# Kernel tuning notes

Measured on AMD Instinct MI355X. Metric: run time of the kernel, lower is better.

## Reference

```python
import jax, jax.numpy as jnp
import numpy as np
import math

KSIZE = 4  # ShortConvolution kernel_size
EPS_NORM = 1e-12
EPS_LN = 1e-5


def short_conv(x, w):
    # x: [b, l, c]; w: [c, K] depthwise causal conv + residual (y = conv(pad(x)) + x)
    b, l, c = x.shape
    K = w.shape[1]
    xp = jnp.pad(x, ((0, 0), (K - 1, 0), (0, 0)))
    y = x  # residual term (x[:, :, K-1:] after padding == x)
    for j in range(K):
        y = y + xp[:, j:j + l, :] * w[:, j]
    return y


def l2norm(x):
    # L2-normalize over last dim (interpreting torch.norm as F.normalize intent)
    return x * jax.lax.rsqrt(jnp.sum(x * x, axis=-1, keepdims=True) + EPS_NORM)


def setup_inputs() -> dict:
    key = jax.random.key(0)
    ks = jax.random.split(key, 12)
    b, l, dim = 4, 2048, 1024
    h = 16
    dk = dim // h
    s = 1.0 / math.sqrt(dim)
    inp = {
        "hidden_states": jax.random.normal(ks[0], (b, l, dim), jnp.float32),
        "Wq": jax.random.normal(ks[1], (dim, dim), jnp.float32) * s,
        "Wk": jax.random.normal(ks[2], (dim, dim), jnp.float32) * s,
        "Wv": jax.random.normal(ks[3], (dim, dim), jnp.float32) * s,
        "conv_q": jax.random.normal(ks[4], (dim, KSIZE), jnp.float32) * 0.1,
        "conv_k": jax.random.normal(ks[5], (dim, KSIZE), jnp.float32) * 0.1,
        "conv_v": jax.random.normal(ks[6], (dim, KSIZE), jnp.float32) * 0.1,
        "W_init": jax.random.normal(ks[7], (1, h, dk, dk), jnp.float32) / math.sqrt(dk),
        "ln_gamma": jnp.ones((dk,), jnp.float32),
        "ln_beta": jnp.zeros((dk,), jnp.float32),
        "Wg": jax.random.normal(ks[8], (dim, dim), jnp.float32) * s,
        "Wo": jax.random.normal(ks[9], (dim, dim), jnp.float32) * s,
    }
    return inp


def titans_forward(hidden_states, Wq, Wk, Wv, conv_q, conv_k, conv_v,
                   W_init, ln_gamma, ln_beta, Wg, Wo,
                   num_heads=16, chunk_size=16):
    b, l, dim = hidden_states.shape
    h = num_heads
    dk = dim // h
    cs = chunk_size
    nc = l // cs

    q = l2norm(jax.nn.silu(short_conv(hidden_states @ Wq.T, conv_q)).reshape(b, l, h, dk))
    k = l2norm(jax.nn.silu(short_conv(hidden_states @ Wk.T, conv_k)).reshape(b, l, h, dk))
    v = jax.nn.silu(short_conv(hidden_states @ Wv.T, conv_v)).reshape(b, l, h, dk)

    # chunked layout: [nc, b, cs, h, d]
    qc = q.reshape(b, nc, cs, h, dk).transpose(1, 0, 2, 3, 4)
    kc = k.reshape(b, nc, cs, h, dk).transpose(1, 0, 2, 3, 4)
    vc = v.reshape(b, nc, cs, h, dk).transpose(1, 0, 2, 3, 4)

    mask = jnp.tril(jnp.ones((cs, cs), q.dtype))
    W0 = jnp.broadcast_to(W_init, (b, h, dk, dk))

    def step(W, chunk):
        q_c, k_c, v_c = chunk
        inter = jnp.einsum('bqhk,bhkv->bqhv', q_c, W)
        qk = jnp.einsum('bqhd,bkhd->bhqk', q_c, k_c) * mask
        intra = jnp.einsum('bhqk,bkhv->bqhv', qk, v_c)
        W_new = W + jnp.einsum('bchk,bchv->bhkv', k_c, v_c)
        return W_new, inter + intra

    _, o = jax.lax.scan(step, W0, (qc, kc, vc))  # o: [nc, b, cs, h, dv]
    o = o.transpose(1, 0, 2, 3, 4).reshape(b, l, h, dk)

    # LayerNorm over head_v_dim
    mu = jnp.mean(o, axis=-1, keepdims=True)
    var = jnp.mean((o - mu) ** 2, axis=-1, keepdims=True)
    o = (o - mu) * jax.lax.rsqrt(var + EPS_LN) * ln_gamma + ln_beta

    o = o.reshape(b, l, dim)
    gate = hidden_states @ Wg.T
    return (o * gate) @ Wo.T


def reference(hidden_states, Wq, Wk, Wv, conv_q, conv_k, conv_v,
              W_init, ln_gamma, ln_beta, Wg, Wo):
    return titans_forward(hidden_states, Wq, Wk, Wv, conv_q, conv_k, conv_v,
                          W_init, ln_gamma, ln_beta, Wg, Wo)
```

## Files before the change

### kernel.cpp

```cpp
#include <hip/hip_runtime.h>

#define L 2048
#define DIM 1024
#define ROWS 8192
#define NSEG 16
#define SEG_CHUNKS 8
#define SEG_TOK 128

typedef __attribute__((ext_vector_type(4))) _Float16 v4h;
typedef __attribute__((ext_vector_type(4))) float v4f;
typedef __attribute__((ext_vector_type(8))) short v8s;

#if defined(__HIP_DEVICE_COMPILE__)
#define MFMA_F16_16x16x16(a, b, c) __builtin_amdgcn_mfma_f32_16x16x16f16((a), (b), (c), 0, 0, 0)
#define MFMA_BF16_16x16x32(a, b, c) __builtin_amdgcn_mfma_f32_16x16x32_bf16((a), (b), (c), 0, 0, 0)
#else
#define MFMA_F16_16x16x16(a, b, c) (c)
#define MFMA_BF16_16x16x32(a, b, c) (c)
#endif

__device__ inline void gld16(const unsigned short* g, unsigned short* l) {
#if defined(__HIP_DEVICE_COMPILE__)
  __builtin_amdgcn_global_load_lds(
      (__attribute__((address_space(1))) void*)g,
      (__attribute__((address_space(3))) void*)l, 16, 0, 0);
#endif
}

__device__ inline unsigned short f2bf(float f) {
  unsigned int u = __float_as_uint(f);
  unsigned int r = (u + 0x7fffu + ((u >> 16) & 1u)) >> 16;
  return (unsigned short)r;
}
__device__ inline void u2_unpack(const uint2 u, float* f) {
  f[0] = __uint_as_float((u.x & 0xffffu) << 16);
  f[1] = __uint_as_float(u.x & 0xffff0000u);
  f[2] = __uint_as_float((u.y & 0xffffu) << 16);
  f[3] = __uint_as_float(u.y & 0xffff0000u);
}
__device__ inline uint4 pack8(const float4 a, const float4 b) {
  uint4 u;
  u.x = (unsigned int)f2bf(a.x) | ((unsigned int)f2bf(a.y) << 16);
  u.y = (unsigned int)f2bf(a.z) | ((unsigned int)f2bf(a.w) << 16);
  u.z = (unsigned int)f2bf(b.x) | ((unsigned int)f2bf(b.y) << 16);
  u.w = (unsigned int)f2bf(b.z) | ((unsigned int)f2bf(b.w) << 16);
  return u;
}
__device__ inline unsigned short f2h_us(float f) {
  _Float16 h = (_Float16)f;
  unsigned short u;
  __builtin_memcpy(&u, &h, 2);
  return u;
}
__device__ inline float h2f_us(unsigned short u) {
  _Float16 h;
  __builtin_memcpy(&h, &u, 2);
  return (float)h;
}
__device__ inline void h4_unpack(const uint2 u, float* f) {
  f[0] = h2f_us((unsigned short)(u.x & 0xffffu));
  f[1] = h2f_us((unsigned short)(u.x >> 16));
  f[2] = h2f_us((unsigned short)(u.y & 0xffffu));
  f[3] = h2f_us((unsigned short)(u.y >> 16));
}

__global__ __launch_bounds__(256) void cvt_f2b(const float* __restrict__ s,
                                               unsigned short* __restrict__ d) {
  const int i = blockIdx.x * 256 + threadIdx.x;
  const float4 v = ((const float4*)s)[i];
  uint2 u;
  u.x = (unsigned int)f2bf(v.x) | ((unsigned int)f2bf(v.y) << 16);
  u.y = (unsigned int)f2bf(v.z) | ((unsigned int)f2bf(v.w) << 16);
  ((uint2*)d)[i] = u;
}

__global__ __launch_bounds__(256) void cvt_w4(const float* __restrict__ w0,
                                              const float* __restrict__ w1,
                                              const float* __restrict__ w2,
                                              const float* __restrict__ w3,
                                              unsigned short* __restrict__ dst) {
  const int t = blockIdx.x >> 10;
  const int i = (blockIdx.x & 1023) * 256 + threadIdx.x;
  const float* s = (t == 0) ? w0 : (t == 1) ? w1 : (t == 2) ? w2 : w3;
  const float4 v = ((const float4*)s)[i];
  uint2 u;
  u.x = (unsigned int)f2bf(v.x) | ((unsigned int)f2bf(v.y) << 16);
  u.y = (unsigned int)f2bf(v.z) | ((unsigned int)f2bf(v.w) << 16);
  ((uint2*)(dst + (size_t)t * DIM * DIM))[i] = u;
}

template <int OUTF32>
__global__ __launch_bounds__(256) void gemm_a(const unsigned short* __restrict__ A,
                                              const unsigned short* __restrict__ B,
                                              void* __restrict__ Cv) {
  __shared__ __align__(16) unsigned short As[128 * 64];
  __shared__ __align__(16) unsigned short Bs[128 * 64];
  const int tid = threadIdx.x;
  const int bm = blockIdx.y * 128;
  const int bn = blockIdx.x * 128;
  const int wave = tid >> 6;
  const int lane = tid & 63;
  const int m16 = lane & 15;
  const int g = lane >> 4;
  const int wm = (wave >> 1) * 64;
  const int wn = (wave & 1) * 64;
  const int srow8 = lane >> 3;
  const int schk = lane & 7;

  v4f acc[4][4];
#pragma unroll
  for (int i = 0; i < 4; i++)
#pragma unroll
    for (int j = 0; j < 4; j++) acc[i][j] = (v4f){0.f, 0.f, 0.f, 0.f};

  for (int kt = 0; kt < DIM; kt += 64) {
    __syncthreads();
#pragma unroll
    for (int j = 0; j < 4; j++) {
      const int r = wave * 32 + j * 8 + srow8;
      const int cg = schk ^ (r & 7);
      gld16(A + (size_t)(bm + r) * DIM + kt + cg * 8, &As[(wave * 32 + j * 8) * 64]);
      gld16(B + (size_t)(bn + r) * DIM + kt + cg * 8, &Bs[(wave * 32 + j * 8) * 64]);
    }
    __syncthreads();
#pragma unroll
    for (int kh = 0; kh < 2; kh++) {
      v8s af[4], bf[4];
#pragma unroll
      for (int i = 0; i < 4; i++) {
        const int r = wm + i * 16 + m16;
        af[i] = *(const v8s*)&As[r * 64 + (((kh * 4 + g) ^ (r & 7)) * 8)];
      }
#pragma unroll
      for (int j = 0; j < 4; j++) {
        const int r = wn + j * 16 + m16;
        bf[j] = *(const v8s*)&Bs[r * 64 + (((kh * 4 + g) ^ (r & 7)) * 8)];
      }
#pragma unroll
      for (int i = 0; i < 4; i++)
#pragma unroll
        for (int j = 0; j < 4; j++) acc[i][j] = MFMA_BF16_16x16x32(af[i], bf[j], acc[i][j]);
    }
  }

  const int t = bn >> 10;
  const int cb = bn & 1023;
#pragma unroll
  for (int i = 0; i < 4; i++)
#pragma unroll
    for (int e = 0; e < 4; e++) {
      const size_t row = (size_t)(bm + wm + i * 16 + 4 * g + e);
#pragma unroll
      for (int j = 0; j < 4; j++) {
        const size_t idx = row * DIM + cb + wn + j * 16 + m16;
        if (OUTF32)
          ((float*)Cv)[idx] = acc[i][j][e];
        else
          ((unsigned short*)Cv)[(size_t)t * ((size_t)ROWS * DIM) + idx] = f2bf(acc[i][j][e]);
      }
    }
}

__global__ __launch_bounds__(256) void gemm_gate(const float* __restrict__ Af,
                                                 const unsigned short* __restrict__ Bf,
                                                 unsigned short* __restrict__ C) {
  __shared__ __align__(16) unsigned short As[128][40];
  __shared__ __align__(16) unsigned short Bs[128][40];
  const int tid = threadIdx.x;
  const int bm = blockIdx.y * 128;
  const int bn = blockIdx.x * 128;
  const int wave = tid >> 6;
  const int lane = tid & 63;
  const int m16 = lane & 15;
  const int g = lane >> 4;
  const int wm = (wave >> 1) * 64;
  const int wn = (wave & 1) * 64;
  const int lr = tid >> 2;
  const int lc = (tid & 3) * 8;

  v4f acc[4][4];
#pragma unroll
  for (int i = 0; i < 4; i++)
#pragma unroll
    for (int j = 0; j < 4; j++) acc[i][j] = (v4f){0.f, 0.f, 0.f, 0.f};

  auto loadAB = [&](int kt, uint4& a0, uint4& a1, uint4& b0, uint4& b1) {
    const float* p0 = Af + (size_t)(bm + lr) * DIM + lc + kt;
    const float* p1 = Af + (size_t)(bm + 64 + lr) * DIM + lc + kt;
    a0 = pack8(*(const float4*)p0, *(const float4*)(p0 + 4));
    a1 = pack8(*(const float4*)p1, *(const float4*)(p1 + 4));
    b0 = *(const uint4*)(Bf + (size_t)(bn + lr) * DIM + lc + kt);
    b1 = *(const uint4*)(Bf + (size_t)(bn + 64 + lr) * DIM + lc + kt);
  };

  uint4 a0, a1, b0, b1;
  loadAB(0, a0, a1, b0, b1);

  for (int kt = 0; kt < DIM; kt += 32) {
    __syncthreads();
    *(uint4*)&As[lr][lc] = a0;
    *(uint4*)&As[64 + lr][lc] = a1;
    *(uint4*)&Bs[lr][lc] = b0;
    *(uint4*)&Bs[64 + lr][lc] = b1;
    __syncthreads();
    if (kt + 32 < DIM) loadAB(kt + 32, a0, a1, b0, b1);
    v8s af[4], bf[4];
#pragma unroll
    for (int i = 0; i < 4; i++) af[i] = *(const v8s*)&As[wm + i * 16 + m16][g * 8];
#pragma unroll
    for (int j = 0; j < 4; j++) bf[j] = *(const v8s*)&Bs[wn + j * 16 + m16][g * 8];
#pragma unroll
    for (int i = 0; i < 4; i++)
#pragma unroll
      for (int j = 0; j < 4; j++) acc[i][j] = MFMA_BF16_16x16x32(af[i], bf[j], acc[i][j]);
  }

#pragma unroll
  for (int i = 0; i < 4; i++)
#pragma unroll
    for (int e = 0; e < 4; e++) {
      const size_t row = (size_t)(bm + wm + i * 16 + 4 * g + e);
#pragma unroll
      for (int j = 0; j < 4; j++)
        C[row * DIM + bn + wn + j * 16 + m16] = f2bf(acc[i][j][e]);
    }
}

__global__ __launch_bounds__(256) void copy_side(const unsigned short* __restrict__ Q,
                                                 const unsigned short* __restrict__ K,
                                                 const unsigned short* __restrict__ V,
                                                 unsigned short* __restrict__ sQ,
                                                 unsigned short* __restrict__ sK,
                                                 unsigned short* __restrict__ sV) {
  const int idx = blockIdx.x;
  const int j = idx % 3;
  const int bs = idx / 3;
  const int seg = bs & 15;
  const int b = bs >> 4;
  const int ch = threadIdx.x * 4;
  const size_t so = ((size_t)(bs * 3 + j)) * DIM + ch;
  if (seg == 0) {
    const uint2 z = {0u, 0u};
    *(uint2*)(sQ + so) = z;
    *(uint2*)(sK + so) = z;
    *(uint2*)(sV + so) = z;
  } else {
    const size_t go = ((size_t)(b * L + seg * SEG_TOK - 3 + j)) * DIM + ch;
    *(uint2*)(sQ + so) = *(const uint2*)(Q + go);
    *(uint2*)(sK + so) = *(const uint2*)(K + go);
    *(uint2*)(sV + so) = *(const uint2*)(V + go);
  }
}

__global__ __launch_bounds__(256) void scan_seg(unsigned short* __restrict__ Qr,
                                                const unsigned short* __restrict__ Kr,
                                                unsigned short* __restrict__ Vr,
                                                const unsigned short* __restrict__ sQ,
                                                const unsigned short* __restrict__ sK,
                                                const unsigned short* __restrict__ sV,
                                                const float* __restrict__ CWq,
                                                const float* __restrict__ CWk,
                                                const float* __restrict__ CWv,
                                                float* __restrict__ D) {
  const int seg = blockIdx.x & 15;
  const int h = (blockIdx.x >> 4) & 15;
  const int b = blockIdx.x >> 8;
  const int tid = threadIdx.x;
  const int lane = tid & 63;
  const int dt = tid >> 6;
  const int m = lane & 15;
  const int g = lane >> 4;
  const int segbase = seg * SEG_TOK;

  __shared__ __align__(16) unsigned short rq[32][68];
  __shared__ __align__(16) unsigned short rk[32][68];
  __shared__ __align__(16) unsigned short rv[32][68];
  __shared__ __align__(16) _Float16 qs[16][72];
  __shared__ __align__(16) _Float16 ks[16][72];
  __shared__ __align__(16) _Float16 kts[64][20];
  __shared__ __align__(16) _Float16 vts[64][20];

  v4f Wf[4];
#pragma unroll
  for (int kt = 0; kt < 4; kt++) Wf[kt] = (v4f){0.f, 0.f, 0.f, 0.f};

  const int srow = tid >> 4;
  const int scol = (tid & 15) * 4;
  const size_t gcol = (size_t)h * 64 + scol;

  float wq[4][4], wk[4][4], wv[4][4];
#pragma unroll
  for (int e = 0; e < 4; e++) {
    const float4 a = *(const float4*)(CWq + (gcol + e) * 4);
    const float4 bw = *(const float4*)(CWk + (gcol + e) * 4);
    const float4 cw = *(const float4*)(CWv + (gcol + e) * 4);
    wq[e][0] = a.x; wq[e][1] = a.y; wq[e][2] = a.z; wq[e][3] = a.w;
    wk[e][0] = bw.x; wk[e][1] = bw.y; wk[e][2] = bw.z; wk[e][3] = bw.w;
    wv[e][0] = cw.x; wv[e][1] = cw.y; wv[e][2] = cw.z; wv[e][3] = cw.w;
  }

  if (tid < 48) {
    const int j = tid >> 4;
    const int sc = (tid & 15) * 4;
    const size_t so = ((size_t)((b * NSEG + seg) * 3 + j)) * DIM + h * 64 + sc;
    const int slot = (29 + j);
    *(uint2*)&rq[slot][sc] = *(const uint2*)(sQ + so);
    *(uint2*)&rk[slot][sc] = *(const uint2*)(sK + so);
    *(uint2*)&rv[slot][sc] = *(const uint2*)(sV + so);
  }

  size_t gb = ((size_t)(b * L + segbase + srow)) * DIM + gcol;
  uint2 qg = *(const uint2*)(Qr + gb);
  uint2 kg = *(const uint2*)(Kr + gb);
  uint2 vg = *(const uint2*)(Vr + gb);

  for (int c = 0; c < SEG_CHUNKS; c++) {
    const int t = segbase + c * 16 + srow;
    __syncthreads();
    *(uint2*)&rq[t & 31][scol] = qg;
    *(uint2*)&rk[t & 31][scol] = kg;
    *(uint2*)&rv[t & 31][scol] = vg;
    const int cn = (c + 1 < SEG_CHUNKS) ? c + 1 : c;
    const size_t gbn = ((size_t)(b * L + segbase + cn * 16 + srow)) * DIM + gcol;
    const uint2 qn = *(const uint2*)(Qr + gbn);
    const uint2 kn = *(const uint2*)(Kr + gbn);
    const uint2 vn = *(const uint2*)(Vr + gbn);
    __syncthreads();

    float sq[4], sk[4], sv[4];
    {
      float q0[4], q1[4], q2[4], q3[4];
      float k0[4], k1[4], k2[4], k3[4];
      float v0[4], v1[4], v2[4], v3[4];
      u2_unpack(qg, q0);
      u2_unpack(kg, k0);
      u2_unpack(vg, v0);
      u2_unpack(*(const uint2*)&rq[(t - 1) & 31][scol], q1);
      u2_unpack(*(const uint2*)&rk[(t - 1) & 31][scol], k1);
      u2_unpack(*(const uint2*)&rv[(t - 1) & 31][scol], v1);
      u2_unpack(*(const uint2*)&rq[(t - 2) & 31][scol], q2);
      u2_unpack(*(const uint2*)&rk[(t - 2) & 31][scol], k2);
      u2_unpack(*(const uint2*)&rv[(t - 2) & 31][scol], v2);
      u2_unpack(*(const uint2*)&rq[(t - 3) & 31][scol], q3);
      u2_unpack(*(const uint2*)&rk[(t - 3) & 31][scol], k3);
      u2_unpack(*(const uint2*)&rv[(t - 3) & 31][scol], v3);
#pragma unroll
      for (int e = 0; e < 4; e++) {
        const float yq = q0[e] + wq[e][0] * q3[e] + wq[e][1] * q2[e] + wq[e][2] * q1[e] + wq[e][3] * q0[e];
        const float yk = k0[e] + wk[e][0] * k3[e] + wk[e][1] * k2[e] + wk[e][2] * k1[e] + wk[e][3] * k0[e];
        const float yv = v0[e] + wv[e][0] * v3[e] + wv[e][1] * v2[e] + wv[e][2] * v1[e] + wv[e][3] * v0[e];
        sq[e] = yq / (1.f + __expf(-yq));
        sk[e] = yk / (1.f + __expf(-yk));
        sv[e] = yv / (1.f + __expf(-yv));
      }
    }
    float ssq = sq[0] * sq[0] + sq[1] * sq[1] + sq[2] * sq[2] + sq[3] * sq[3];
    float ssk = sk[0] * sk[0] + sk[1] * sk[1] + sk[2] * sk[2] + sk[3] * sk[3];
#pragma unroll
    for (int off = 8; off >= 1; off >>= 1) {
      ssq += __shfl_xor(ssq, off, 16);
      ssk += __shfl_xor(ssk, off, 16);
    }
    const float scq = rsqrtf(ssq + 1e-12f);
    const float sck = rsqrtf(ssk + 1e-12f);

    const v4h qh = {(_Float16)(sq[0] * scq), (_Float16)(sq[1] * scq),
                    (_Float16)(sq[2] * scq), (_Float16)(sq[3] * scq)};
    const v4h kh = {(_Float16)(sk[0] * sck), (_Float16)(sk[1] * sck),
                    (_Float16)(sk[2] * sck), (_Float16)(sk[3] * sck)};
    *(v4h*)&qs[srow][scol] = qh;
    *(v4h*)&ks[srow][scol] = kh;
    kts[scol + 0][srow] = kh[0]; kts[scol + 1][srow] = kh[1];
    kts[scol + 2][srow] = kh[2]; kts[scol + 3][srow] = kh[3];
    vts[scol + 0][srow] = (_Float16)sv[0]; vts[scol + 1][srow] = (_Float16)sv[1];
    vts[scol + 2][srow] = (_Float16)sv[2]; vts[scol + 3][srow] = (_Float16)sv[3];

    uint2 qp;
    __builtin_memcpy(&qp, &qh, 8);
    *(uint2*)(Qr + gb) = qp;

    __syncthreads();

    v4h qf[4], kf[4], ktf[4];
#pragma unroll
    for (int kt = 0; kt < 4; kt++) {
      qf[kt] = *(const v4h*)&qs[m][kt * 16 + 4 * g];
      kf[kt] = *(const v4h*)&ks[m][kt * 16 + 4 * g];
      ktf[kt] = *(const v4h*)&kts[kt * 16 + m][4 * g];
    }
    const v4h vf = *(const v4h*)&vts[dt * 16 + m][4 * g];

    v4f kq = {0.f, 0.f, 0.f, 0.f};
#pragma unroll
    for (int kt = 0; kt < 4; kt++) kq = MFMA_F16_16x16x16(kf[kt], qf[kt], kq);

    v4h kqA;
#pragma unroll
    for (int e = 0; e < 4; e++)
      kqA[e] = (4 * g + e <= m) ? (_Float16)kq[e] : (_Float16)0.f;

    v4f of = {0.f, 0.f, 0.f, 0.f};
    of = MFMA_F16_16x16x16(kqA, vf, of);
#pragma unroll
    for (int kt = 0; kt < 4; kt++) {
      v4h Wh;
#pragma unroll
      for (int e = 0; e < 4; e++) Wh[e] = (_Float16)Wf[kt][e];
      of = MFMA_F16_16x16x16(qf[kt], Wh, of);
    }
#pragma unroll
    for (int kt = 0; kt < 4; kt++) Wf[kt] = MFMA_F16_16x16x16(ktf[kt], vf, Wf[kt]);

    const size_t ob = ((size_t)(b * L + segbase + c * 16 + 4 * g)) * DIM + h * 64 + dt * 16 + m;
#pragma unroll
    for (int e = 0; e < 4; e++) Vr[ob + (size_t)e * DIM] = f2h_us(of[e]);

    qg = qn; kg = kn; vg = vn; gb = gbn;
  }

  float* Dp = D + ((size_t)((b * 16 + h) * NSEG + seg)) * 4096;
#pragma unroll
  for (int kt = 0; kt < 4; kt++)
#pragma unroll
    for (int e = 0; e < 4; e++)
      Dp[(kt * 16 + 4 * g + e) * 64 + dt * 16 + m] = Wf[kt][e];
}

__global__ __launch_bounds__(256) void prefix_D(float* __restrict__ D,
                                                const float* __restrict__ W0) {
  const int bh = blockIdx.x;
  const int h = bh & 15;
  const int tid = threadIdx.x;
  float p[16];
#pragma unroll
  for (int i = 0; i < 16; i++) p[i] = W0[(size_t)h * 4096 + tid + i * 256];
  for (int s = 0; s < NSEG; s++) {
    float* Dp = D + ((size_t)bh * NSEG + s) * 4096;
#pragma unroll
    for (int i = 0; i < 16; i++) {
      const float t = Dp[tid + i * 256];
      Dp[tid + i * 256] = p[i];
      p[i] += t;
    }
  }
}

__global__ __launch_bounds__(256) void apply_corr(const unsigned short* __restrict__ Qc,
                                                  const float* __restrict__ P,
                                                  unsigned short* __restrict__ Op) {
  const int seg = blockIdx.x & 15;
  const int h = (blockIdx.x >> 4) & 15;
  const int b = blockIdx.x >> 8;
  const int tid = threadIdx.x;
  const int lane = tid & 63;
  const int dt = tid >> 6;
  const int m = lane & 15;
  const int g = lane >> 4;

  __shared__ __align__(16) _Float16 Pt[64][72];
  __shared__ __align__(16) _Float16 qt[16][72];

  const float* Pp = P + ((size_t)((b * 16 + h) * NSEG + seg)) * 4096;
#pragma unroll
  for (int i = 0; i < 16; i++) {
    const int el = tid + i * 256;
    Pt[el & 63][el >> 6] = (_Float16)Pp[el];
  }
  __syncthreads();

  v4h pb[4];
#pragma unroll
  for (int kt = 0; kt < 4; kt++) pb[kt] = *(const v4h*)&Pt[dt * 16 + m][kt * 16 + 4 * g];

  const int srow = tid >> 4;
  const int scol = (tid & 15) * 4;
  for (int rt = 0; rt < 8; rt++) {
    const size_t gb = ((size_t)(b * L + seg * SEG_TOK + rt * 16 + srow)) * DIM + h * 64 + scol;
    const uint2 qg = *(const uint2*)(Qc + gb);
    __syncthreads();
    *(uint2*)&qt[srow][scol] = qg;
    __syncthreads();
    v4h qf[4];
#pragma unroll
    for (int kt = 0; kt < 4; kt++) qf[kt] = *(const v4h*)&qt[m][kt * 16 + 4 * g];
    v4f corr = {0.f, 0.f, 0.f, 0.f};
#pragma unroll
    for (int kt = 0; kt < 4; kt++) corr = MFMA_F16_16x16x16(qf[kt], pb[kt], corr);
    const size_t ob = ((size_t)(b * L + seg * SEG_TOK + rt * 16 + 4 * g)) * DIM + h * 64 + dt * 16 + m;
#pragma unroll
    for (int e = 0; e < 4; e++) {
      const float v = h2f_us(Op[ob + (size_t)e * DIM]) + corr[e];
      Op[ob + (size_t)e * DIM] = f2h_us(v);
    }
  }
}

__global__ __launch_bounds__(256) void ln_gate(unsigned short* __restrict__ Ob,
                                               const unsigned short* __restrict__ G,
                                               const float* __restrict__ gamma,
                                               const float* __restrict__ beta) {
  const int r = blockIdx.x;
  const int tid = threadIdx.x;
  const int c = tid * 4;
  float o[4];
  h4_unpack(*(const uint2*)(Ob + (size_t)r * DIM + c), o);
  float sum = o[0] + o[1] + o[2] + o[3];
#pragma unroll
  for (int off = 8; off >= 1; off >>= 1) sum += __shfl_xor(sum, off, 16);
  const float mu = sum * (1.f / 64.f);
  float d[4];
  float vs = 0.f;
#pragma unroll
  for (int e = 0; e < 4; e++) { d[e] = o[e] - mu; vs += d[e] * d[e]; }
#pragma unroll
  for (int off = 8; off >= 1; off >>= 1) vs += __shfl_xor(vs, off, 16);
  const float rstd = rsqrtf(vs * (1.f / 64.f) + 1e-5f);
  const int dl = c & 63;
  const float4 gm = *(const float4*)(gamma + dl);
  const float4 bt = *(const float4*)(beta + dl);
  float gt[4];
  u2_unpack(*(const uint2*)(G + (size_t)r * DIM + c), gt);
  float outv[4];
  outv[0] = (d[0] * rstd * gm.x + bt.x) * gt[0];
  outv[1] = (d[1] * rstd * gm.y + bt.y) * gt[1];
  outv[2] = (d[2] * rstd * gm.z + bt.z) * gt[2];
  outv[3] = (d[3] * rstd * gm.w + bt.w) * gt[3];
  uint2 u;
  u.x = (unsigned int)f2bf(outv[0]) | ((unsigned int)f2bf(outv[1]) << 16);
  u.y = (unsigned int)f2bf(outv[2]) | ((unsigned int)f2bf(outv[3]) << 16);
  *(uint2*)(Ob + (size_t)r * DIM + c) = u;
}

extern "C" void kernel_launch(void* const* d_in, const int* in_sizes, int n_in,
                              void* d_out, int out_size, void* d_ws, size_t ws_size,
                              hipStream_t stream) {
  const float* H  = (const float*)d_in[0];
  const float* Wq = (const float*)d_in[1];
  const float* Wk = (const float*)d_in[2];
  const float* Wv = (const float*)d_in[3];
  const float* cq = (const float*)d_in[4];
  const float* ck = (const float*)d_in[5];
  const float* cv = (const float*)d_in[6];
  const float* W0 = (const float*)d_in[7];
  const float* gamma = (const float*)d_in[8];
  const float* beta  = (const float*)d_in[9];
  const float* Wg = (const float*)d_in[10];
  const float* Wo = (const float*)d_in[11];

  const size_t SZ = (size_t)ROWS * DIM;
  const size_t WSZ = (size_t)DIM * DIM;
  unsigned short* sA = (unsigned short*)d_ws;
  unsigned short* sB = sA + SZ;
  unsigned short* sC = sB + SZ;

  unsigned short* Hbf = (unsigned short*)d_out;
  unsigned short* Wbf = Hbf + SZ;
  unsigned short* side = Wbf + 4 * WSZ;
  unsigned short* sideQ = side;
  unsigned short* sideK = side + (size_t)192 * DIM;
  unsigned short* sideV = side + (size_t)384 * DIM;
  float* D = (float*)d_out;

  cvt_f2b<<<SZ / 1024, 256, 0, stream>>>(H, Hbf);
  cvt_w4<<<4096, 256, 0, stream>>>(Wq, Wk, Wv, Wg, Wbf);

  gemm_a<0><<<dim3(24, 64), 256, 0, stream>>>(Hbf, Wbf, sA);

  copy_side<<<192, 256, 0, stream>>>(sA, sB, sC, sideQ, sideK, sideV);

  scan_seg<<<1024, 256, 0, stream>>>(sA, sB, sC, sideQ, sideK, sideV,
                                     cq, ck, cv, D);

  gemm_gate<<<dim3(8, 64), 256, 0, stream>>>(H, Wbf + 3 * WSZ, sB);

  prefix_D<<<64, 256, 0, stream>>>(D, W0);

  apply_corr<<<1024, 256, 0, stream>>>(sA, D, sC);

  ln_gate<<<ROWS, 256, 0, stream>>>(sC, sB, gamma, beta);

  cvt_f2b<<<WSZ / 1024, 256, 0, stream>>>(Wo, sA);

  gemm_a<1><<<dim3(8, 64), 256, 0, stream>>>(sC, sA, d_out);
}
```

Baseline: 323.7 us.

## Fuse gate GEMM into QKV GEMM, merge conversions, fuse correction with LayerNorm-gate

Merges the input and weight bf16 conversions into one kernel. When workspace is large enough, computes the gate projection as a fourth output tile group of the bf16 QKV GEMM instead of a separate fp32-input GEMM. Fuses the inter-segment correction with the LayerNorm and gating step, staging corrected outputs in shared memory so the O tensor is not re-read by a separate kernel. This adds more barriers per tile and a workspace-size-dependent code path.

```diff
diff --git a/kernel.cpp b/kernel.cpp
--- a/kernel.cpp
+++ b/kernel.cpp
@@ -62,6 +62,33 @@
   f[1] = h2f_us((unsigned short)(u.x >> 16));
   f[2] = h2f_us((unsigned short)(u.y & 0xffffu));
   f[3] = h2f_us((unsigned short)(u.y >> 16));
+}
+
+__global__ __launch_bounds__(256) void cvt_all(const float* __restrict__ H,
+                                               const float* __restrict__ w0,
+                                               const float* __restrict__ w1,
+                                               const float* __restrict__ w2,
+                                               const float* __restrict__ w3,
+                                               unsigned short* __restrict__ Hbf,
+                                               unsigned short* __restrict__ Wbf) {
+  const int i = blockIdx.x * 256 + threadIdx.x;
+  const float* s;
+  unsigned short* d;
+  int li;
+  if (i < 2097152) {
+    s = H; d = Hbf; li = i;
+  } else {
+    const int j = i - 2097152;
+    const int w = j >> 18;
+    li = j & 262143;
+    s = (w == 0) ? w0 : (w == 1) ? w1 : (w == 2) ? w2 : w3;
+    d = Wbf + (size_t)w * DIM * DIM;
+  }
+  const float4 v = ((const float4*)s)[li];
+  uint2 u;
+  u.x = (unsigned int)f2bf(v.x) | ((unsigned int)f2bf(v.y) << 16);
+  u.y = (unsigned int)f2bf(v.z) | ((unsigned int)f2bf(v.w) << 16);
+  ((uint2*)d)[li] = u;
 }
 
 __global__ __launch_bounds__(256) void cvt_f2b(const float* __restrict__ s,
@@ -74,25 +101,13 @@
   ((uint2*)d)[i] = u;
 }
 
-__global__ __launch_bounds__(256) void cvt_w4(const float* __restrict__ w0,
-                                              const float* __restrict__ w1,
-                                              const float* __restrict__ w2,
-                                              const float* __restrict__ w3,
-                                              unsigned short* __restrict__ dst) {
-  const int t = blockIdx.x >> 10;
-  const int i = (blockIdx.x & 1023) * 256 + threadIdx.x;
-  const float* s = (t == 0) ? w0 : (t == 1) ? w1 : (t == 2) ? w2 : w3;
-  const float4 v = ((const float4*)s)[i];
-  uint2 u;
-  u.x = (unsigned int)f2bf(v.x) | ((unsigned int)f2bf(v.y) << 16);
-  u.y = (unsigned int)f2bf(v.z) | ((unsigned int)f2bf(v.w) << 16);
-  ((uint2*)(dst + (size_t)t * DIM * DIM))[i] = u;
-}
-
 template <int OUTF32>
 __global__ __launch_bounds__(256) void gemm_a(const unsigned short* __restrict__ A,
                                               const unsigned short* __restrict__ B,
-                                              void* __restrict__ Cv) {
+                                              unsigned short* __restrict__ o0,
+                                              unsigned short* __restrict__ o1,
+                                              unsigned short* __restrict__ o2,
+                                              unsigned short* __restrict__ o3) {
   __shared__ __align__(16) unsigned short As[128 * 64];
   __shared__ __align__(16) unsigned short Bs[128 * 64];
   const int tid = threadIdx.x;
@@ -145,6 +160,7 @@
 
   const int t = bn >> 10;
   const int cb = bn & 1023;
+  unsigned short* C = (t == 0) ? o0 : (t == 1) ? o1 : (t == 2) ? o2 : o3;
 #pragma unroll
   for (int i = 0; i < 4; i++)
 #pragma unroll
@@ -154,9 +170,9 @@
       for (int j = 0; j < 4; j++) {
         const size_t idx = row * DIM + cb + wn + j * 16 + m16;
         if (OUTF32)
-          ((float*)Cv)[idx] = acc[i][j][e];
+          ((float*)o0)[idx] = acc[i][j][e];
         else
-          ((unsigned short*)Cv)[(size_t)t * ((size_t)ROWS * DIM) + idx] = f2bf(acc[i][j][e]);
+          C[idx] = f2bf(acc[i][j][e]);
       }
     }
 }
@@ -445,9 +461,12 @@
   }
 }
 
-__global__ __launch_bounds__(256) void apply_corr(const unsigned short* __restrict__ Qc,
-                                                  const float* __restrict__ P,
-                                                  unsigned short* __restrict__ Op) {
+__global__ __launch_bounds__(256) void corr_ln_gate(const unsigned short* __restrict__ Qc,
+                                                    const float* __restrict__ P,
+                                                    unsigned short* __restrict__ Op,
+                                                    const unsigned short* __restrict__ G,
+                                                    const float* __restrict__ gamma,
+                                                    const float* __restrict__ beta) {
   const int seg = blockIdx.x & 15;
   const int h = (blockIdx.x >> 4) & 15;
   const int b = blockIdx.x >> 8;
@@ -459,6 +478,7 @@
 
   __shared__ __align__(16) _Float16 Pt[64][72];
   __shared__ __align__(16) _Float16 qt[16][72];
+  __shared__ __align__(16) float ot[16][68];
 
   const float* Pp = P + ((size_t)((b * 16 + h) * NSEG + seg)) * 4096;
 #pragma unroll
@@ -474,8 +494,12 @@
 
   const int srow = tid >> 4;
   const int scol = (tid & 15) * 4;
+  const float4 gm = *(const float4*)(gamma + scol);
+  const float4 bt = *(const float4*)(beta + scol);
+
   for (int rt = 0; rt < 8; rt++) {
-    const size_t gb = ((size_t)(b * L + seg * SEG_TOK + rt * 16 + srow)) * DIM + h * 64 + scol;
+    const int row0 = seg * SEG_TOK + rt * 16;
+    const size_t gb = ((size_t)(b * L + row0 + srow)) * DIM + h * 64 + scol;
     const uint2 qg = *(const uint2*)(Qc + gb);
     __syncthreads();
     *(uint2*)&qt[srow][scol] = qg;
@@ -486,49 +510,33 @@
     v4f corr = {0.f, 0.f, 0.f, 0.f};
 #pragma unroll
     for (int kt = 0; kt < 4; kt++) corr = MFMA_F16_16x16x16(qf[kt], pb[kt], corr);
-    const size_t ob = ((size_t)(b * L + seg * SEG_TOK + rt * 16 + 4 * g)) * DIM + h * 64 + dt * 16 + m;
-#pragma unroll
-    for (int e = 0; e < 4; e++) {
-      const float v = h2f_us(Op[ob + (size_t)e * DIM]) + corr[e];
-      Op[ob + (size_t)e * DIM] = f2h_us(v);
-    }
-  }
-}
-
-__global__ __launch_bounds__(256) void ln_gate(unsigned short* __restrict__ Ob,
-                                               const unsigned short* __restrict__ G,
-                                               const float* __restrict__ gamma,
-                                               const float* __restrict__ beta) {
-  const int r = blockIdx.x;
-  const int tid = threadIdx.x;
-  const int c = tid * 4;
-  float o[4];
-  h4_unpack(*(const uint2*)(Ob + (size_t)r * DIM + c), o);
-  float sum = o[0] + o[1] + o[2] + o[3];
-#pragma unroll
-  for (int off = 8; off >= 1; off >>= 1) sum += __shfl_xor(sum, off, 16);
-  const float mu = sum * (1.f / 64.f);
-  float d[4];
-  float vs = 0.f;
-#pragma unroll
-  for (int e = 0; e < 4; e++) { d[e] = o[e] - mu; vs += d[e] * d[e]; }
-#pragma unroll
-  for (int off = 8; off >= 1; off >>= 1) vs += __shfl_xor(vs, off, 16);
-  const float rstd = rsqrtf(vs * (1.f / 64.f) + 1e-5f);
-  const int dl = c & 63;
-  const float4 gm = *(const float4*)(gamma + dl);
-  const float4 bt = *(const float4*)(beta + dl);
-  float gt[4];
-  u2_unpack(*(const uint2*)(G + (size_t)r * DIM + c), gt);
-  float outv[4];
-  outv[0] = (d[0] * rstd * gm.x + bt.x) * gt[0];
-  outv[1] = (d[1] * rstd * gm.y + bt.y) * gt[1];
-  outv[2] = (d[2] * rstd * gm.z + bt.z) * gt[2];
-  outv[3] = (d[3] * rstd * gm.w + bt.w) * gt[3];
-  uint2 u;
-  u.x = (unsigned int)f2bf(outv[0]) | ((unsigned int)f2bf(outv[1]) << 16);
-  u.y = (unsigned int)f2bf(outv[2]) | ((unsigned int)f2bf(outv[3]) << 16);
-  *(uint2*)(Ob + (size_t)r * DIM + c) = u;
+    const size_t ob = ((size_t)(b * L + row0 + 4 * g)) * DIM + h * 64 + dt * 16 + m;
+#pragma unroll
+    for (int e = 0; e < 4; e++)
+      ot[4 * g + e][dt * 16 + m] = h2f_us(Op[ob + (size_t)e * DIM]) + corr[e];
+    __syncthreads();
+    const float4 ov = *(const float4*)&ot[srow][scol];
+    float sum = ov.x + ov.y + ov.z + ov.w;
+#pragma unroll
+    for (int off = 8; off >= 1; off >>= 1) sum += __shfl_xor(sum, off, 16);
+    const float mu = sum * (1.f / 64.f);
+    const float d0 = ov.x - mu, d1 = ov.y - mu, d2 = ov.z - mu, d3 = ov.w - mu;
+    float vs = d0 * d0 + d1 * d1 + d2 * d2 + d3 * d3;
+#pragma unroll
+    for (int off = 8; off >= 1; off >>= 1) vs += __shfl_xor(vs, off, 16);
+    const float rstd = rsqrtf(vs * (1.f / 64.f) + 1e-5f);
+    float gt[4];
+    u2_unpack(*(const uint2*)(G + gb), gt);
+    float outv[4];
+    outv[0] = (d0 * rstd * gm.x + bt.x) * gt[0];
+    outv[1] = (d1 * rstd * gm.y + bt.y) * gt[1];
+    outv[2] = (d2 * rstd * gm.z + bt.z) * gt[2];
+    outv[3] = (d3 * rstd * gm.w + bt.w) * gt[3];
+    uint2 u;
+    u.x = (unsigned int)f2bf(outv[0]) | ((unsigned int)f2bf(outv[1]) << 16);
+    u.y = (unsigned int)f2bf(outv[2]) | ((unsigned int)f2bf(outv[3]) << 16);
+    *(uint2*)(Op + gb) = u;
+  }
 }
 
 extern "C" void kernel_launch(void* const* d_in, const int* in_sizes, int n_in,
@@ -549,37 +557,45 @@
 
   const size_t SZ = (size_t)ROWS * DIM;
   const size_t WSZ = (size_t)DIM * DIM;
+  const size_t SIDE = (size_t)192 * DIM;
   unsigned short* sA = (unsigned short*)d_ws;
   unsigned short* sB = sA + SZ;
   unsigned short* sC = sB + SZ;
 
+  const bool bigws = ws_size >= (3 * SZ + 4 * WSZ + 3 * SIDE) * 2;
+
   unsigned short* Hbf = (unsigned short*)d_out;
-  unsigned short* Wbf = Hbf + SZ;
-  unsigned short* side = Wbf + 4 * WSZ;
-  unsigned short* sideQ = side;
-  unsigned short* sideK = side + (size_t)192 * DIM;
-  unsigned short* sideV = side + (size_t)384 * DIM;
   float* D = (float*)d_out;
 
-  cvt_f2b<<<SZ / 1024, 256, 0, stream>>>(H, Hbf);
-  cvt_w4<<<4096, 256, 0, stream>>>(Wq, Wk, Wv, Wg, Wbf);
-
-  gemm_a<0><<<dim3(24, 64), 256, 0, stream>>>(Hbf, Wbf, sA);
-
-  copy_side<<<192, 256, 0, stream>>>(sA, sB, sC, sideQ, sideK, sideV);
-
-  scan_seg<<<1024, 256, 0, stream>>>(sA, sB, sC, sideQ, sideK, sideV,
-                                     cq, ck, cv, D);
-
-  gemm_gate<<<dim3(8, 64), 256, 0, stream>>>(H, Wbf + 3 * WSZ, sB);
-
-  prefix_D<<<64, 256, 0, stream>>>(D, W0);
-
-  apply_corr<<<1024, 256, 0, stream>>>(sA, D, sC);
-
-  ln_gate<<<ROWS, 256, 0, stream>>>(sC, sB, gamma, beta);
-
-  cvt_f2b<<<WSZ / 1024, 256, 0, stream>>>(Wo, sA);
-
-  gemm_a<1><<<dim3(8, 64), 256, 0, stream>>>(sC, sA, d_out);
-}
+  if (bigws) {
+    unsigned short* Wbf = sC + SZ;
+    unsigned short* side = Wbf + 4 * WSZ;
+    unsigned short* gate = Hbf + SZ;
+
+    cvt_all<<<12288, 256, 0, stream>>>(H, Wq, Wk, Wv, Wg, Hbf, Wbf);
+    gemm_a<0><<<dim3(32, 64), 256, 0, stream>>>(Hbf, Wbf, sA, sB, sC, gate);
+    copy_side<<<192, 256, 0, stream>>>(sA, sB, sC, side, side + SIDE, side + 2 * SIDE);
+    scan_seg<<<1024, 256, 0, stream>>>(sA, sB, sC, side, side + SIDE, side + 2 * SIDE,
+                                       cq, ck, cv, D);
+    prefix_D<<<64, 256, 0, stream>>>(D, W0);
+    corr_ln_gate<<<1024, 256, 0, stream>>>(sA, D, sC, gate, gamma, beta);
+    cvt_f2b<<<WSZ / 1024, 256, 0, stream>>>(Wo, sA);
+    gemm_a<1><<<dim3(8, 64), 256, 0, stream>>>(sC, sA, (unsigned short*)d_out,
+                                               nullptr, nullptr, nullptr);
+  } else {
+    unsigned short* Wbf = Hbf + SZ;
+    unsigned short* side = Wbf + 4 * WSZ;
+
+    cvt_all<<<12288, 256, 0, stream>>>(H, Wq, Wk, Wv, Wg, Hbf, Wbf);
+    gemm_a<0><<<dim3(24, 64), 256, 0, stream>>>(Hbf, Wbf, sA, sB, sC, nullptr);
+    copy_side<<<192, 256, 0, stream>>>(sA, sB, sC, side, side + SIDE, side + 2 * SIDE);
+    scan_seg<<<1024, 256, 0, stream>>>(sA, sB, sC, side, side + SIDE, side + 2 * SIDE,
+                                       cq, ck, cv, D);
+    gemm_gate<<<dim3(8, 64), 256, 0, stream>>>(H, Wbf + 3 * WSZ, sB);
+    prefix_D<<<64, 256, 0, stream>>>(D, W0);
+    corr_ln_gate<<<1024, 256, 0, stream>>>(sA, D, sC, sB, gamma, beta);
+    cvt_f2b<<<WSZ / 1024, 256, 0, stream>>>(Wo, sA);
+    gemm_a<1><<<dim3(8, 64), 256, 0, stream>>>(sC, sA, (unsigned short*)d_out,
+                                               nullptr, nullptr, nullptr);
+  }
+}
```

Result: faster. 287.7 us (-11.1%).
